# Kernel optimization log

Hardware: AMD Instinct MI355X
Metric: run time of the kernel (lower is better)

Reference implementation:

```python
import jax, jax.numpy as jnp
import numpy as np

B, S, D, H = 1, 2048, 4096, 32
HD = D // H
THETA = 10000.0
IN_SCALE = 0.1   # input_scale buffer
Q_SCALE = 0.1    # q_proj_scale buffer
K_SCALE = 0.1    # k_proj_scale buffer
V_SCALE = 0.1    # v_proj_scale buffer
OUT_SCALE = 0.1  # out_input_scale buffer


def _fake_q(x, scale, lo, hi):
    # round-to-int + clamp, kept in float (faithful to int8 fake-quant)
    return jnp.clip(jnp.round(x / scale), lo, hi)


def _w4a8_linear(x, qw, w_scale, in_scale):
    # int8 fake-quantized activation x int4-valued weight, dequant output
    qx = _fake_q(x, in_scale, -128, 127)
    return jnp.einsum('bsd,od->bso', qx, qw) * (in_scale * w_scale)


def _rope_tables(position_ids):
    inv_freq = 1.0 / (THETA ** (jnp.arange(0, HD, 2, dtype=jnp.float32) / HD))
    ang = position_ids.astype(jnp.float32)[..., None] * inv_freq  # [B,S,HD/2]
    emb = jnp.concatenate([ang, ang], axis=-1)                     # [B,S,HD]
    return jnp.cos(emb)[:, None], jnp.sin(emb)[:, None]            # [B,1,S,HD]


def _rotate_half(x):
    return jnp.concatenate([-x[..., HD // 2:], x[..., :HD // 2]], axis=-1)


def setup_inputs() -> dict:
    key = jax.random.key(0)
    ks = jax.random.split(key, 9)
    hidden_states = jax.random.normal(ks[0], (B, S, D), jnp.float32)
    def int4_w(k):
        return jnp.round(jax.random.uniform(k, (D, D), jnp.float32, -8.0, 7.0))
    def ch_scale(k):
        return jax.random.uniform(k, (D,), jnp.float32, 0.01, 0.03)
    wq, wk, wv, wo = int4_w(ks[1]), int4_w(ks[2]), int4_w(ks[3]), int4_w(ks[4])
    sq_w, sk_w, sv_w, so_w = ch_scale(ks[5]), ch_scale(ks[6]), ch_scale(ks[7]), ch_scale(ks[8])
    position_ids = jnp.arange(S, dtype=jnp.int32)[None, :]
    causal = jnp.tril(jnp.ones((S, S), dtype=bool))
    attention_mask = jnp.where(causal, 0.0, -1e9).astype(jnp.float32)[None, None]
    return dict(hidden_states=hidden_states, wq=wq, wk=wk, wv=wv, wo=wo,
                sq_w=sq_w, sk_w=sk_w, sv_w=sv_w, so_w=so_w,
                attention_mask=attention_mask, position_ids=position_ids)


def reference(hidden_states, wq, wk, wv, wo, sq_w, sk_w, sv_w, so_w,
              attention_mask, position_ids):
    # W4A8 dequant projections
    q = _w4a8_linear(hidden_states, wq, sq_w, IN_SCALE)
    k = _w4a8_linear(hidden_states, wk, sk_w, IN_SCALE)
    v = _w4a8_linear(hidden_states, wv, sv_w, IN_SCALE)
    q = q.reshape(B, S, H, HD).transpose(0, 2, 1, 3)  # [B,H,S,HD]
    k = k.reshape(B, S, H, HD).transpose(0, 2, 1, 3)
    v = v.reshape(B, S, H, HD).transpose(0, 2, 1, 3)
    # RoPE
    cos, sin = _rope_tables(position_ids)
    q = q * cos + _rotate_half(q) * sin
    k = k * cos + _rotate_half(k) * sin
    # int8 fake-quant of q/k/v, then dequant before matmuls
    q = _fake_q(q, Q_SCALE, -128, 127)
    k = _fake_q(k, K_SCALE, -128, 127)
    v = _fake_q(v, V_SCALE, -128, 127)
    scores = jnp.einsum('bhqd,bhkd->bhqk', q * Q_SCALE, k * K_SCALE) / np.sqrt(HD)
    scores = scores + attention_mask
    attn = jax.nn.softmax(scores.astype(jnp.float32), axis=-1)
    out = jnp.einsum('bhqk,bhkd->bhqd', attn, v * V_SCALE)
    out = out.transpose(0, 2, 1, 3).reshape(B, S, D)
    # o_proj input re-quantized to int8 with out_input_scale (clamp -127..127)
    out_q = _fake_q(out, OUT_SCALE, -127, 127)
    attn_output = jnp.einsum('bsd,od->bso', out_q, wo) * (OUT_SCALE * so_w)
    return attn_output
```

## Files before the change

### kernel.cpp

```cpp
#include <hip/hip_runtime.h>
#include <math.h>
#include <stdint.h>

#define S_LEN 2048
#define D_DIM 4096
#define NHEAD 32
#define HDIM  128

typedef int      v4i __attribute__((ext_vector_type(4)));
typedef float    v4f __attribute__((ext_vector_type(4)));
typedef _Float16 v8h __attribute__((ext_vector_type(8)));

__device__ __forceinline__ float quant128(float x) {
  return fminf(fmaxf(rintf(x / 0.1f), -128.f), 127.f);
}
__device__ __forceinline__ void gl_lds16(const void* g, void* l) {
  __builtin_amdgcn_global_load_lds(
      (const __attribute__((address_space(1))) void*)g,
      (__attribute__((address_space(3))) void*)l, 16, 0, 0);
}

__global__ __launch_bounds__(256) void quant_hidden_k(const float* __restrict__ in,
                                                      int8_t* __restrict__ out) {
  const int idx = blockIdx.x * 256 + threadIdx.x;
  const float4 v = ((const float4*)in)[idx];
  const int q0 = (int)quant128(v.x), q1 = (int)quant128(v.y);
  const int q2 = (int)quant128(v.z), q3 = (int)quant128(v.w);
  ((int*)out)[idx] = (q0 & 0xff) | ((q1 & 0xff) << 8) | ((q2 & 0xff) << 16) | ((q3 & 0xff) << 24);
}

__global__ __launch_bounds__(256) void wconv3_k(const float* __restrict__ a,
                                                const float* __restrict__ b,
                                                const float* __restrict__ c,
                                                int8_t* __restrict__ out) {
  const int which = blockIdx.x >> 14;
  const int sub = blockIdx.x & 16383;
  const float* src = (which == 0) ? a : (which == 1) ? b : c;
  const int idx = sub * 256 + threadIdx.x;
  const float4 v = ((const float4*)src)[idx];
  const int q0 = __float2int_rn(v.x), q1 = __float2int_rn(v.y);
  const int q2 = __float2int_rn(v.z), q3 = __float2int_rn(v.w);
  ((int*)out)[(size_t)which * 4194304 + idx] =
      (q0 & 0xff) | ((q1 & 0xff) << 8) | ((q2 & 0xff) << 16) | ((q3 & 0xff) << 24);
}

__global__ __launch_bounds__(256) void wconv_k(const float* __restrict__ in,
                                               int8_t* __restrict__ out) {
  const int idx = blockIdx.x * 256 + threadIdx.x;
  const float4 v = ((const float4*)in)[idx];
  const int q0 = __float2int_rn(v.x), q1 = __float2int_rn(v.y);
  const int q2 = __float2int_rn(v.z), q3 = __float2int_rn(v.w);
  ((int*)out)[idx] = (q0 & 0xff) | ((q1 & 0xff) << 8) | ((q2 & 0xff) << 16) | ((q3 & 0xff) << 24);
}

__global__ __launch_bounds__(256) void rope_tab_k(const int* __restrict__ pos,
                                                  float* __restrict__ ct,
                                                  float* __restrict__ st) {
  const int idx = blockIdx.x * 256 + threadIdx.x;
  const int s = idx >> 6, j = idx & 63;
  const float inv = exp2f((float)j * -0.20762050593046016f);
  const float a = (float)pos[s] * inv;
  float si, c;
  sincosf(a, &si, &c);
  ct[idx] = c;
  st[idx] = si;
}

template <int MODE>
__global__ __launch_bounds__(512, 1) void gemm8p(
    const int8_t* __restrict__ A8, const int8_t* __restrict__ W8,
    const float* __restrict__ s0, const float* __restrict__ s1,
    const float* __restrict__ s2, const float* __restrict__ ctab,
    const float* __restrict__ stab, void* __restrict__ out0,
    void* __restrict__ out1, void* __restrict__ out2) {
  __shared__ __align__(16) int8_t LS[3 * 16384 + 3 * 32768];
  int8_t* const Abase = LS;
  int8_t* const Bbase = LS + 49152;

  const int t = threadIdx.x;
  const int w = t >> 6, lane = t & 63, g = lane >> 4, l15 = lane & 15;
  const int wm = w >> 2, wn = w & 3;

  const int G = blockIdx.x;
  const int within = G & 15, g16 = G >> 4;
  const int bm = ((g16 & 3) * 4 + (within >> 2)) * 128;
  const int bn = ((g16 >> 2) * 4 + (within & 3)) * 256;

  const int rowo = lane >> 3;
  const int schunk = ((lane & 7) ^ rowo) * 16;
  const int8_t* srcA[2];
  const int8_t* srcB[4];
#pragma unroll
  for (int i = 0; i < 2; ++i)
    srcA[i] = A8 + (size_t)(bm + w * 16 + i * 8 + rowo) * D_DIM + schunk;
#pragma unroll
  for (int i = 0; i < 4; ++i)
    srcB[i] = W8 + (size_t)(bn + w * 32 + i * 8 + rowo) * D_DIM + schunk;

#define STAGE(KT, BI)                                                       \
  {                                                                         \
    const int kof_ = (KT) * 128;                                            \
    int8_t* Ad_ = Abase + (BI) * 16384 + w * 2048;                          \
    int8_t* Bd_ = Bbase + (BI) * 32768 + w * 4096;                          \
    _Pragma("unroll") for (int i_ = 0; i_ < 2; ++i_)                        \
        gl_lds16(srcA[i_] + kof_, Ad_ + i_ * 1024);                         \
    _Pragma("unroll") for (int i_ = 0; i_ < 4; ++i_)                        \
        gl_lds16(srcB[i_] + kof_, Bd_ + i_ * 1024);                         \
  }

  const int nc0 = (wn & 1) * 32 + (wn >> 1) * 128;

  v4i acc[4][4];
#pragma unroll
  for (int mi = 0; mi < 4; ++mi)
#pragma unroll
    for (int ni = 0; ni < 4; ++ni) acc[mi][ni] = (v4i){0, 0, 0, 0};

  STAGE(0, 0)
  STAGE(1, 1)

  for (int t3 = 0; t3 < 33; t3 += 3) {
#pragma unroll
    for (int u = 0; u < 3; ++u) {
      const int kt = t3 + u;
      if (kt < 32) {
        if (kt + 1 < 32)
          asm volatile("s_waitcnt vmcnt(6)" ::: "memory");
        else
          asm volatile("s_waitcnt vmcnt(0)" ::: "memory");
        __builtin_amdgcn_s_barrier();
        if (kt + 2 < 32) STAGE(kt + 2, ((u + 2) % 3))
        const int8_t* Ab = Abase + u * 16384;
        const int8_t* Bb = Bbase + u * 32768;
#pragma unroll
        for (int kk = 0; kk < 2; ++kk) {
          const int coff = (((kk << 2) | g) ^ (l15 & 7)) * 16;
          v4i bf[4], af[4];
#pragma unroll
          for (int ni = 0; ni < 4; ++ni) {
            const int nrow = nc0 + (ni & 1) * 16 + (ni >> 1) * 64 + l15;
            bf[ni] = *(const v4i*)(Bb + nrow * 128 + coff);
          }
#pragma unroll
          for (int mi = 0; mi < 4; ++mi)
            af[mi] = *(const v4i*)(Ab + (wm * 64 + mi * 16 + l15) * 128 + coff);
          __builtin_amdgcn_s_setprio(1);
#pragma unroll
          for (int mi = 0; mi < 4; ++mi)
#pragma unroll
            for (int ni = 0; ni < 4; ++ni)
              acc[mi][ni] =
                  __builtin_amdgcn_mfma_i32_16x16x64_i8(af[mi], bf[ni], acc[mi][ni], 0, 0, 0);
          __builtin_amdgcn_s_setprio(0);
        }
      }
    }
  }
#undef STAGE

  const int srow0 = bm + wm * 64;
  if (MODE == 1) {
    float* dst = (float*)out0;
#pragma unroll
    for (int ni = 0; ni < 4; ++ni) {
      const int col = bn + nc0 + (ni & 1) * 16 + (ni >> 1) * 64 + l15;
      const float sc = 0.1f * s0[col];
#pragma unroll
      for (int mi = 0; mi < 4; ++mi)
#pragma unroll
        for (int r = 0; r < 4; ++r)
          dst[(size_t)(srow0 + mi * 16 + g * 4 + r) * D_DIM + col] =
              (float)acc[mi][ni][r] * sc;
    }
  } else {
    const int seg = bn >> 12;
    const int bcol = bn & 4095;
    if (seg == 2) {
      _Float16* dst = (_Float16*)out2;
#pragma unroll
      for (int ni = 0; ni < 4; ++ni) {
        const int col = bcol + nc0 + (ni & 1) * 16 + (ni >> 1) * 64 + l15;
        const float scv = 0.1f * s2[col];
#pragma unroll
        for (int mi = 0; mi < 4; ++mi)
#pragma unroll
          for (int r = 0; r < 4; ++r) {
            const int s = srow0 + mi * 16 + g * 4 + r;
            dst[(size_t)col * S_LEN + s] = (_Float16)quant128((float)acc[mi][ni][r] * scv);
          }
      }
    } else {
      const float* wsc = seg ? s1 : s0;
      int8_t* dst = seg ? (int8_t*)out1 : (int8_t*)out0;
      const int hb = bcol + (wn >> 1) * 128;
#pragma unroll
      for (int ni = 0; ni < 2; ++ni) {
        const int dlo = (wn & 1) * 32 + ni * 16 + l15;
        const int clo = hb + dlo;
        const float sc0 = 0.1f * wsc[clo];
        const float sc1 = 0.1f * wsc[clo + 64];
#pragma unroll
        for (int mi = 0; mi < 4; ++mi)
#pragma unroll
          for (int r = 0; r < 4; ++r) {
            const int s = srow0 + mi * 16 + g * 4 + r;
            const float c = ctab[s * 64 + dlo];
            const float si = stab[s * 64 + dlo];
            const float x1 = (float)acc[mi][ni][r] * sc0;
            const float x2 = (float)acc[mi][ni + 2][r] * sc1;
            dst[(size_t)s * D_DIM + clo] = (int8_t)quant128(x1 * c - x2 * si);
            dst[(size_t)s * D_DIM + clo + 64] = (int8_t)quant128(x2 * c + x1 * si);
          }
      }
    }
  }
}

__global__ __launch_bounds__(256, 3) void attn_v5(
    const int8_t* __restrict__ q8, const int8_t* __restrict__ k8,
    const _Float16* __restrict__ vT, int8_t* __restrict__ o8) {
  __shared__ __align__(16) int8_t Kls[2][8192];
  __shared__ __align__(16) int8_t Vls[2][16384];
  const int j = 31 - blockIdx.x;
  const int h = blockIdx.y;
  const int t = threadIdx.x;
  const int w = t >> 6, lane = t & 63, g = lane >> 4, l15 = lane & 15;
  const int T = j + 1;
  const int q0 = (4 * j + w) * 16;
  const int q_lane = q0 + l15;
  const float SSCALE = 8.838834764831845e-4f;
  const v8h vones = {(_Float16)1, (_Float16)1, (_Float16)1, (_Float16)1,
                     (_Float16)1, (_Float16)1, (_Float16)1, (_Float16)1};

  int k_src[2], v_src[4], kv_dst[4];
#pragma unroll
  for (int i = 0; i < 2; ++i) {
    const int lin = i * 256 + t;
    const int s = lin >> 3;
    const int cs = (lin & 7) ^ (s & 7);
    const int key = ((s >> 5) & 1) * 32 + ((s >> 3) & 1) * 16 +
                    ((s >> 2) & 1) * 8 + ((s >> 4) & 1) * 4 + (s & 3);
    k_src[i] = key * D_DIM + cs * 16;
  }
#pragma unroll
  for (int i = 0; i < 4; ++i) {
    const int lin = i * 256 + t;
    const int d = lin >> 3;
    const int cs = (lin & 7) ^ (d & 7);
    v_src[i] = d * S_LEN + cs * 8;
    kv_dst[i] = lin * 16;
  }
  const int8_t* kbg = k8 + (size_t)h * HDIM;
  const _Float16* vbg = vT + (size_t)h * HDIM * S_LEN;

  auto stage = [&](int kt, int b) {
    const int8_t* ks = kbg + (size_t)kt * (64 * D_DIM);
    const _Float16* vs = vbg + kt * 64;
#pragma unroll
    for (int i = 0; i < 2; ++i) gl_lds16(ks + k_src[i], Kls[b] + kv_dst[i]);
#pragma unroll
    for (int i = 0; i < 4; ++i) gl_lds16(vs + v_src[i], Vls[b] + kv_dst[i]);
  };

  const v4i qa0 = *(const v4i*)(q8 + (size_t)q_lane * D_DIM + h * HDIM + g * 16);
  const v4i qa1 = *(const v4i*)(q8 + (size_t)q_lane * D_DIM + h * HDIM + 64 + g * 16);

  v4f o[8];
#pragma unroll
  for (int n = 0; n < 8; ++n) o[n] = (v4f){0.f, 0.f, 0.f, 0.f};
  v4f lacc = (v4f){0.f, 0.f, 0.f, 0.f};
  float m_i = -INFINITY;

  stage(0, 0);

  for (int kt = 0; kt < T; ++kt) {
    const int b = kt & 1;
    __syncthreads();
    if (kt + 1 < T) stage(kt + 1, b ^ 1);

    const int ksw = (l15 & 7);
    float sc[4][4];
#pragma unroll
    for (int nt = 0; nt < 4; ++nt) {
      const int8_t* kr = Kls[b] + (nt * 16 + l15) * 128;
      const v4i kb0 = *(const v4i*)(kr + ((g ^ ksw) * 16));
      const v4i kb1 = *(const v4i*)(kr + (((4 + g) ^ ksw) * 16));
      v4i c = (v4i){0, 0, 0, 0};
      c = __builtin_amdgcn_mfma_i32_16x16x64_i8(kb0, qa0, c, 0, 0, 0);
      c = __builtin_amdgcn_mfma_i32_16x16x64_i8(kb1, qa1, c, 0, 0, 0);
#pragma unroll
      for (int r = 0; r < 4; ++r) {
        float s = (float)c[r] * SSCALE;
        if (kt == T - 1) {
          const int key = kt * 64 + ((nt >> 1) << 5) + ((g >> 1) << 4) +
                          ((g & 1) << 3) + ((nt & 1) << 2) + r;
          if (key > q_lane) s = -1.0e30f;
        }
        sc[nt][r] = s;
      }
    }
    float mx = fmaxf(fmaxf(fmaxf(sc[0][0], sc[0][1]), fmaxf(sc[0][2], sc[0][3])),
                     fmaxf(fmaxf(sc[1][0], sc[1][1]), fmaxf(sc[1][2], sc[1][3])));
    mx = fmaxf(mx, fmaxf(fmaxf(fmaxf(sc[2][0], sc[2][1]), fmaxf(sc[2][2], sc[2][3])),
                         fmaxf(fmaxf(sc[3][0], sc[3][1]), fmaxf(sc[3][2], sc[3][3]))));
    mx = fmaxf(mx, __shfl_xor(mx, 16));
    mx = fmaxf(mx, __shfl_xor(mx, 32));
    const float mnew = fmaxf(m_i, mx);
    const float alpha = __expf(m_i - mnew);
    m_i = mnew;

    float p[4][4];
#pragma unroll
    for (int nt = 0; nt < 4; ++nt)
#pragma unroll
      for (int r = 0; r < 4; ++r) p[nt][r] = __expf(sc[nt][r] - m_i);

    v8h ph0, ph1;
#pragma unroll
    for (int e = 0; e < 8; ++e) {
      ph0[e] = (_Float16)p[e >> 2][e & 3];
      ph1[e] = (_Float16)p[2 + (e >> 2)][e & 3];
    }
    float a_r[4];
#pragma unroll
    for (int r = 0; r < 4; ++r)
      a_r[r] = __shfl(alpha, (lane & 48) | (g * 4 + r));
#pragma unroll
    for (int n = 0; n < 8; ++n)
#pragma unroll
      for (int r = 0; r < 4; ++r) o[n][r] *= a_r[r];
#pragma unroll
    for (int r = 0; r < 4; ++r) lacc[r] *= a_r[r];

    __builtin_amdgcn_s_setprio(1);
    lacc = __builtin_amdgcn_mfma_f32_16x16x32_f16(ph0, vones, lacc, 0, 0, 0);
    lacc = __builtin_amdgcn_mfma_f32_16x16x32_f16(ph1, vones, lacc, 0, 0, 0);
#pragma unroll
    for (int nt = 0; nt < 8; ++nt) {
      const int8_t* vr = Vls[b] + (nt * 16 + l15) * 128;
      const v8h v0 = *(const v8h*)(vr + ((g ^ ksw) * 16));
      const v8h v1 = *(const v8h*)(vr + (((4 + g) ^ ksw) * 16));
      o[nt] = __builtin_amdgcn_mfma_f32_16x16x32_f16(ph0, v0, o[nt], 0, 0, 0);
      o[nt] = __builtin_amdgcn_mfma_f32_16x16x32_f16(ph1, v1, o[nt], 0, 0, 0);
    }
    __builtin_amdgcn_s_setprio(0);
  }

#pragma unroll
  for (int r = 0; r < 4; ++r) {
    const float rL = 1.0f / lacc[r];
    const size_t row = (size_t)(q0 + g * 4 + r) * D_DIM + h * HDIM;
#pragma unroll
    for (int nt = 0; nt < 8; ++nt) {
      const int q = (int)fminf(fmaxf(rintf(o[nt][r] * rL), -127.f), 127.f);
      o8[row + nt * 16 + l15] = (int8_t)q;
    }
  }
}

extern "C" void kernel_launch(void* const* d_in, const int* in_sizes, int n_in,
                              void* d_out, int out_size, void* d_ws, size_t ws_size,
                              hipStream_t stream) {
  (void)in_sizes; (void)n_in; (void)out_size; (void)ws_size;
  const float* hidden = (const float*)d_in[0];
  const float* wq = (const float*)d_in[1];
  const float* wk = (const float*)d_in[2];
  const float* wv = (const float*)d_in[3];
  const float* wo = (const float*)d_in[4];
  const float* sq = (const float*)d_in[5];
  const float* sk = (const float*)d_in[6];
  const float* sv = (const float*)d_in[7];
  const float* so = (const float*)d_in[8];
  const int* pos = (const int*)d_in[10];
  float* out = (float*)d_out;

  char* ws = (char*)d_ws;
  int8_t* h8 = (int8_t*)ws;
  int8_t* q8 = (int8_t*)(ws + (8ull << 20));
  int8_t* k8 = (int8_t*)(ws + (16ull << 20));
  _Float16* vT = (_Float16*)(ws + (24ull << 20));
  int8_t* w8a = (int8_t*)(ws + (40ull << 20));
  int8_t* w8b = (int8_t*)(ws + (56ull << 20));
  int8_t* w8c = (int8_t*)(ws + (72ull << 20));
  float* ctab = (float*)(ws + (88ull << 20));
  float* stab = (float*)(ws + (88ull << 20) + (512ull << 10));
  int8_t* o8 = h8;

  hipLaunchKernelGGL(rope_tab_k, dim3(512), dim3(256), 0, stream, pos, ctab, stab);
  hipLaunchKernelGGL(quant_hidden_k, dim3(8192), dim3(256), 0, stream, hidden, h8);
  hipLaunchKernelGGL(wconv3_k, dim3(49152), dim3(256), 0, stream, wq, wk, wv, w8a);

  hipLaunchKernelGGL((gemm8p<0>), dim3(768), dim3(512), 0, stream, h8, w8a,
                     sq, sk, sv, ctab, stab, (void*)q8, (void*)k8, (void*)vT);
  hipLaunchKernelGGL(wconv_k, dim3(16384), dim3(256), 0, stream, wo, w8a);
  hipLaunchKernelGGL(attn_v5, dim3(32, 32), dim3(256), 0, stream, q8, k8, vT, o8);
  hipLaunchKernelGGL((gemm8p<1>), dim3(256), dim3(512), 0, stream, o8, w8a,
                     so, so, so, ctab, stab, (void*)out, (void*)out, (void*)out);
}
```

Before: 518.9 us.

## Triple-buffer K in LDS, load V directly to registers, XCD-remap GEMM blocks

The attention kernel now stages only K through a three-deep LDS ring with explicit vmcnt waits and a bare barrier. V tiles are loaded straight from global memory into registers, split into two halves so their latency overlaps the QK MFMAs. The GEMM kernels remap block indices across the eight XCDs to improve L2 locality. This cuts LDS traffic and footprint, at the cost of more register pressure and uncoalesced-ish global V reads.

```diff
diff --git a/kernel.cpp b/kernel.cpp
--- a/kernel.cpp
+++ b/kernel.cpp
@@ -81,8 +81,10 @@
   const int w = t >> 6, lane = t & 63, g = lane >> 4, l15 = lane & 15;
   const int wm = w >> 2, wn = w & 3;
 
-  const int G = blockIdx.x;
-  const int within = G & 15, g16 = G >> 4;
+  const int nwg = gridDim.x;
+  const int bid = blockIdx.x;
+  const int lb = (bid & 7) * (nwg >> 3) + (bid >> 3);
+  const int within = lb & 15, g16 = lb >> 4;
   const int bm = ((g16 & 3) * 4 + (within >> 2)) * 128;
   const int bn = ((g16 >> 2) * 4 + (within & 3)) * 256;
 
@@ -216,11 +218,10 @@
   }
 }
 
-__global__ __launch_bounds__(256, 3) void attn_v5(
+__global__ __launch_bounds__(256, 3) void attn_v6(
     const int8_t* __restrict__ q8, const int8_t* __restrict__ k8,
     const _Float16* __restrict__ vT, int8_t* __restrict__ o8) {
-  __shared__ __align__(16) int8_t Kls[2][8192];
-  __shared__ __align__(16) int8_t Vls[2][16384];
+  __shared__ __align__(16) int8_t Kls[3][8192];
   const int j = 31 - blockIdx.x;
   const int h = blockIdx.y;
   const int t = threadIdx.x;
@@ -232,7 +233,7 @@
   const v8h vones = {(_Float16)1, (_Float16)1, (_Float16)1, (_Float16)1,
                      (_Float16)1, (_Float16)1, (_Float16)1, (_Float16)1};
 
-  int k_src[2], v_src[4], kv_dst[4];
+  int k_src[2], k_dst[2];
 #pragma unroll
   for (int i = 0; i < 2; ++i) {
     const int lin = i * 256 + t;
@@ -241,25 +242,15 @@
     const int key = ((s >> 5) & 1) * 32 + ((s >> 3) & 1) * 16 +
                     ((s >> 2) & 1) * 8 + ((s >> 4) & 1) * 4 + (s & 3);
     k_src[i] = key * D_DIM + cs * 16;
-  }
-#pragma unroll
-  for (int i = 0; i < 4; ++i) {
-    const int lin = i * 256 + t;
-    const int d = lin >> 3;
-    const int cs = (lin & 7) ^ (d & 7);
-    v_src[i] = d * S_LEN + cs * 8;
-    kv_dst[i] = lin * 16;
+    k_dst[i] = lin * 16;
   }
   const int8_t* kbg = k8 + (size_t)h * HDIM;
   const _Float16* vbg = vT + (size_t)h * HDIM * S_LEN;
 
-  auto stage = [&](int kt, int b) {
+  auto stageK = [&](int kt, int bi) {
     const int8_t* ks = kbg + (size_t)kt * (64 * D_DIM);
-    const _Float16* vs = vbg + kt * 64;
-#pragma unroll
-    for (int i = 0; i < 2; ++i) gl_lds16(ks + k_src[i], Kls[b] + kv_dst[i]);
-#pragma unroll
-    for (int i = 0; i < 4; ++i) gl_lds16(vs + v_src[i], Vls[b] + kv_dst[i]);
+#pragma unroll
+    for (int i = 0; i < 2; ++i) gl_lds16(ks + k_src[i], &Kls[bi][k_dst[i]]);
   };
 
   const v4i qa0 = *(const v4i*)(q8 + (size_t)q_lane * D_DIM + h * HDIM + g * 16);
@@ -271,18 +262,30 @@
   v4f lacc = (v4f){0.f, 0.f, 0.f, 0.f};
   float m_i = -INFINITY;
 
-  stage(0, 0);
-
+  stageK(0, 0);
+  if (T > 1) stageK(1, 1);
+
+  int bi = 0;
   for (int kt = 0; kt < T; ++kt) {
-    const int b = kt & 1;
-    __syncthreads();
-    if (kt + 1 < T) stage(kt + 1, b ^ 1);
+    if (kt + 1 < T)
+      asm volatile("s_waitcnt vmcnt(2)" ::: "memory");
+    else
+      asm volatile("s_waitcnt vmcnt(0)" ::: "memory");
+    __builtin_amdgcn_s_barrier();
+
+    v8h va0[4], va1[4];
+#pragma unroll
+    for (int nt = 0; nt < 4; ++nt) {
+      const _Float16* vp = vbg + (size_t)(nt * 16 + l15) * S_LEN + kt * 64 + g * 8;
+      va0[nt] = *(const v8h*)vp;
+      va1[nt] = *(const v8h*)(vp + 32);
+    }
 
     const int ksw = (l15 & 7);
     float sc[4][4];
 #pragma unroll
     for (int nt = 0; nt < 4; ++nt) {
-      const int8_t* kr = Kls[b] + (nt * 16 + l15) * 128;
+      const int8_t* kr = &Kls[bi][(nt * 16 + l15) * 128];
       const v4i kb0 = *(const v4i*)(kr + ((g ^ ksw) * 16));
       const v4i kb1 = *(const v4i*)(kr + (((4 + g) ^ ksw) * 16));
       v4i c = (v4i){0, 0, 0, 0};
@@ -299,6 +302,17 @@
         sc[nt][r] = s;
       }
     }
+
+    v8h vb0[4], vb1[4];
+#pragma unroll
+    for (int nt = 0; nt < 4; ++nt) {
+      const _Float16* vp =
+          vbg + (size_t)((nt + 4) * 16 + l15) * S_LEN + kt * 64 + g * 8;
+      vb0[nt] = *(const v8h*)vp;
+      vb1[nt] = *(const v8h*)(vp + 32);
+    }
+    if (kt + 2 < T) stageK(kt + 2, bi ? bi - 1 : 2);
+
     float mx = fmaxf(fmaxf(fmaxf(sc[0][0], sc[0][1]), fmaxf(sc[0][2], sc[0][3])),
                      fmaxf(fmaxf(sc[1][0], sc[1][1]), fmaxf(sc[1][2], sc[1][3])));
     mx = fmaxf(mx, fmaxf(fmaxf(fmaxf(sc[2][0], sc[2][1]), fmaxf(sc[2][2], sc[2][3])),
@@ -336,14 +350,18 @@
     lacc = __builtin_amdgcn_mfma_f32_16x16x32_f16(ph0, vones, lacc, 0, 0, 0);
     lacc = __builtin_amdgcn_mfma_f32_16x16x32_f16(ph1, vones, lacc, 0, 0, 0);
 #pragma unroll
-    for (int nt = 0; nt < 8; ++nt) {
-      const int8_t* vr = Vls[b] + (nt * 16 + l15) * 128;
-      const v8h v0 = *(const v8h*)(vr + ((g ^ ksw) * 16));
-      const v8h v1 = *(const v8h*)(vr + (((4 + g) ^ ksw) * 16));
-      o[nt] = __builtin_amdgcn_mfma_f32_16x16x32_f16(ph0, v0, o[nt], 0, 0, 0);
-      o[nt] = __builtin_amdgcn_mfma_f32_16x16x32_f16(ph1, v1, o[nt], 0, 0, 0);
+    for (int nt = 0; nt < 4; ++nt) {
+      o[nt] = __builtin_amdgcn_mfma_f32_16x16x32_f16(ph0, va0[nt], o[nt], 0, 0, 0);
+      o[nt] = __builtin_amdgcn_mfma_f32_16x16x32_f16(ph1, va1[nt], o[nt], 0, 0, 0);
+    }
+#pragma unroll
+    for (int nt = 0; nt < 4; ++nt) {
+      o[nt + 4] = __builtin_amdgcn_mfma_f32_16x16x32_f16(ph0, vb0[nt], o[nt + 4], 0, 0, 0);
+      o[nt + 4] = __builtin_amdgcn_mfma_f32_16x16x32_f16(ph1, vb1[nt], o[nt + 4], 0, 0, 0);
     }
     __builtin_amdgcn_s_setprio(0);
+
+    bi = (bi == 2) ? 0 : bi + 1;
   }
 
 #pragma unroll
@@ -393,7 +411,7 @@
   hipLaunchKernelGGL((gemm8p<0>), dim3(768), dim3(512), 0, stream, h8, w8a,
                      sq, sk, sv, ctab, stab, (void*)q8, (void*)k8, (void*)vT);
   hipLaunchKernelGGL(wconv_k, dim3(16384), dim3(256), 0, stream, wo, w8a);
-  hipLaunchKernelGGL(attn_v5, dim3(32, 32), dim3(256), 0, stream, q8, k8, vT, o8);
+  hipLaunchKernelGGL(attn_v6, dim3(32, 32), dim3(256), 0, stream, q8, k8, vT, o8);
   hipLaunchKernelGGL((gemm8p<1>), dim3(256), dim3(512), 0, stream, o8, w8a,
                      so, so, so, ctab, stab, (void*)out, (void*)out, (void*)out);
 }
```

After: 716.4 us. 1.38x slower.

## Triple-buffer attention K/V loads and remap GEMM workgroups across XCDs

Applied to the files above, without the earlier changes.

The attention kernel moves from double to triple buffering of K/V tiles in LDS. It prefetches two tiles ahead and uses explicit vmcnt waits plus a raw barrier in place of __syncthreads, so global loads overlap more compute. LDS use rises to 72KB, so occupancy drops from 3 to 2 blocks per CU. The GEMM remaps block IDs so consecutive logical tiles land on the same XCD for better L2 reuse, and adds a sched_barrier after the pipeline barrier.

```diff
diff --git a/kernel.cpp b/kernel.cpp
--- a/kernel.cpp
+++ b/kernel.cpp
@@ -81,8 +81,10 @@
   const int w = t >> 6, lane = t & 63, g = lane >> 4, l15 = lane & 15;
   const int wm = w >> 2, wn = w & 3;
 
-  const int G = blockIdx.x;
-  const int within = G & 15, g16 = G >> 4;
+  const int nwg = gridDim.x;
+  const int bid = blockIdx.x;
+  const int lb = (bid & 7) * (nwg >> 3) + (bid >> 3);
+  const int within = lb & 15, g16 = lb >> 4;
   const int bm = ((g16 & 3) * 4 + (within >> 2)) * 128;
   const int bn = ((g16 >> 2) * 4 + (within & 3)) * 256;
 
@@ -129,6 +131,7 @@
         else
           asm volatile("s_waitcnt vmcnt(0)" ::: "memory");
         __builtin_amdgcn_s_barrier();
+        __builtin_amdgcn_sched_barrier(0);
         if (kt + 2 < 32) STAGE(kt + 2, ((u + 2) % 3))
         const int8_t* Ab = Abase + u * 16384;
         const int8_t* Bb = Bbase + u * 32768;
@@ -216,11 +219,11 @@
   }
 }
 
-__global__ __launch_bounds__(256, 3) void attn_v5(
+__global__ __launch_bounds__(256, 2) void attn_v7(
     const int8_t* __restrict__ q8, const int8_t* __restrict__ k8,
     const _Float16* __restrict__ vT, int8_t* __restrict__ o8) {
-  __shared__ __align__(16) int8_t Kls[2][8192];
-  __shared__ __align__(16) int8_t Vls[2][16384];
+  __shared__ __align__(16) int8_t Kls[3][8192];
+  __shared__ __align__(16) int8_t Vls[3][16384];
   const int j = 31 - blockIdx.x;
   const int h = blockIdx.y;
   const int t = threadIdx.x;
@@ -257,9 +260,9 @@
     const int8_t* ks = kbg + (size_t)kt * (64 * D_DIM);
     const _Float16* vs = vbg + kt * 64;
 #pragma unroll
-    for (int i = 0; i < 2; ++i) gl_lds16(ks + k_src[i], Kls[b] + kv_dst[i]);
-#pragma unroll
-    for (int i = 0; i < 4; ++i) gl_lds16(vs + v_src[i], Vls[b] + kv_dst[i]);
+    for (int i = 0; i < 2; ++i) gl_lds16(ks + k_src[i], &Kls[b][kv_dst[i]]);
+#pragma unroll
+    for (int i = 0; i < 4; ++i) gl_lds16(vs + v_src[i], &Vls[b][kv_dst[i]]);
   };
 
   const v4i qa0 = *(const v4i*)(q8 + (size_t)q_lane * D_DIM + h * HDIM + g * 16);
@@ -272,17 +275,23 @@
   float m_i = -INFINITY;
 
   stage(0, 0);
-
+  if (T > 1) stage(1, 1);
+
+  int bi = 0;
   for (int kt = 0; kt < T; ++kt) {
-    const int b = kt & 1;
-    __syncthreads();
-    if (kt + 1 < T) stage(kt + 1, b ^ 1);
+    if (kt + 1 < T)
+      asm volatile("s_waitcnt vmcnt(6)" ::: "memory");
+    else
+      asm volatile("s_waitcnt vmcnt(0)" ::: "memory");
+    __builtin_amdgcn_s_barrier();
+    __builtin_amdgcn_sched_barrier(0);
+    if (kt + 2 < T) stage(kt + 2, bi >= 1 ? bi - 1 : bi + 2);
 
     const int ksw = (l15 & 7);
     float sc[4][4];
 #pragma unroll
     for (int nt = 0; nt < 4; ++nt) {
-      const int8_t* kr = Kls[b] + (nt * 16 + l15) * 128;
+      const int8_t* kr = &Kls[bi][(nt * 16 + l15) * 128];
       const v4i kb0 = *(const v4i*)(kr + ((g ^ ksw) * 16));
       const v4i kb1 = *(const v4i*)(kr + (((4 + g) ^ ksw) * 16));
       v4i c = (v4i){0, 0, 0, 0};
@@ -337,13 +346,15 @@
     lacc = __builtin_amdgcn_mfma_f32_16x16x32_f16(ph1, vones, lacc, 0, 0, 0);
 #pragma unroll
     for (int nt = 0; nt < 8; ++nt) {
-      const int8_t* vr = Vls[b] + (nt * 16 + l15) * 128;
+      const int8_t* vr = &Vls[bi][(nt * 16 + l15) * 128];
       const v8h v0 = *(const v8h*)(vr + ((g ^ ksw) * 16));
       const v8h v1 = *(const v8h*)(vr + (((4 + g) ^ ksw) * 16));
       o[nt] = __builtin_amdgcn_mfma_f32_16x16x32_f16(ph0, v0, o[nt], 0, 0, 0);
       o[nt] = __builtin_amdgcn_mfma_f32_16x16x32_f16(ph1, v1, o[nt], 0, 0, 0);
     }
     __builtin_amdgcn_s_setprio(0);
+
+    bi = (bi == 2) ? 0 : bi + 1;
   }
 
 #pragma unroll
@@ -393,7 +404,7 @@
   hipLaunchKernelGGL((gemm8p<0>), dim3(768), dim3(512), 0, stream, h8, w8a,
                      sq, sk, sv, ctab, stab, (void*)q8, (void*)k8, (void*)vT);
   hipLaunchKernelGGL(wconv_k, dim3(16384), dim3(256), 0, stream, wo, w8a);
-  hipLaunchKernelGGL(attn_v5, dim3(32, 32), dim3(256), 0, stream, q8, k8, vT, o8);
+  hipLaunchKernelGGL(attn_v7, dim3(32, 32), dim3(256), 0, stream, q8, k8, vT, o8);
   hipLaunchKernelGGL((gemm8p<1>), dim3(256), dim3(512), 0, stream, o8, w8a,
                      so, so, so, ctab, stab, (void*)out, (void*)out, (void*)out);
 }
```

Measured after the change: 523.0 us. No clear change (+0.8%).
